# Optimization experiments

Measured on AMD Instinct MI355X. Metric: run time of the kernel, lower is better.

## Reference

```python
import jax, jax.numpy as jnp
import numpy as np

B, F, V, D, K = 16384, 39, 30000, 16, 20
EPS = 1e-5


def bn_eval(x, g, b):
    # inference-mode BatchNorm1d with running_mean=0, running_var=1
    return g * x / jnp.sqrt(1.0 + EPS) + b


def setup_inputs() -> dict:
    key = jax.random.key(0)
    ks = jax.random.split(key, 12)
    x = jax.random.randint(ks[0], (B, F), 0, V)
    emb_table = jax.random.normal(ks[1], (F * V, D), dtype=jnp.float32) * 0.05
    w_c = jax.random.normal(ks[2], (F, F * D), dtype=jnp.float32) * 0.05
    w0 = jax.random.normal(ks[3], (1024, F * D), dtype=jnp.float32) * 0.04
    w1 = jax.random.normal(ks[4], (512, 1024), dtype=jnp.float32) * 0.03
    w_out = jax.random.normal(ks[5], (1, 512), dtype=jnp.float32) * 0.04
    return {
        'x': x, 'emb_table': emb_table,
        'w_c': w_c, 'b_c': jnp.zeros((F,)), 'g_c': jnp.ones((F,)), 'be_c': jnp.zeros((F,)),
        'w0': w0, 'b0': jnp.zeros((1024,)), 'g0': jnp.ones((1024,)), 'be0': jnp.zeros((1024,)),
        'w1': w1, 'b1': jnp.zeros((512,)), 'g1': jnp.ones((512,)), 'be1': jnp.zeros((512,)),
        'w_out': w_out, 'b_out': jnp.zeros((1,)),
    }


def reference(x, emb_table, w_c, b_c, g_c, be_c, w0, b0, g0, be0,
              w1, b1, g1, be1, w_out, b_out):
    offsets = jnp.arange(F, dtype=x.dtype) * V          # per-field offsets
    idx = x + offsets[None, :]                          # [B, F]
    emb = emb_table[idx]                                # [B, F, D] gather

    # controller_mlp: flatten (batch, D, F) layout like torch transpose(1,2)
    flat = jnp.transpose(emb, (0, 2, 1)).reshape(B, F * D)
    h = jax.nn.relu(bn_eval(flat @ w_c.T + b_c, g_c, be_c))
    scores = jax.nn.softmax(h, axis=1)                  # [B, F]

    # kmax_pooling: top-k field indices, sorted ascending, gather weights
    _, kidx = jax.lax.top_k(scores, K)
    kidx = jnp.sort(kidx, axis=1)                       # [B, K]
    w = jnp.take_along_axis(scores, kidx, axis=1)       # [B, K]

    # forward_select: gather selected field embeddings, weight them
    sel = jnp.take_along_axis(emb, kidx[:, :, None], axis=1)  # [B, K, D]
    weighted = sel * w[:, :, None]

    # scatter back into full field slots (unselected fields are zero)
    full = jnp.zeros((B, F, D), weighted.dtype)
    bidx = jnp.arange(B)[:, None]
    full = full.at[bidx, kidx].set(weighted)            # [B, F, D]

    z = jnp.transpose(full, (0, 2, 1)).reshape(B, F * D)
    z = jax.nn.relu(bn_eval(z @ w0.T + b0, g0, be0))
    z = jax.nn.relu(bn_eval(z @ w1.T + b1, g1, be1))
    out = jax.nn.sigmoid(z @ w_out.T + b_out)           # [B, 1]
    return out.squeeze(-1)
```

## Files before the change

### kernel.cpp

```cpp
#include <hip/hip_runtime.h>
#include <math.h>

#define B_SZ 16384
#define F_N 39
#define V_N 30000
#define D_N 16
#define K_SEL 20
#define FD 624
#define KP0 640
#define NCP 48
#define N0 1024
#define N1 512
#define CBR 16
#define ALD 648

typedef unsigned short u16;
typedef __attribute__((ext_vector_type(8))) short bf16x8;
typedef __attribute__((ext_vector_type(8))) unsigned short u16x8;
typedef __attribute__((ext_vector_type(4))) float f32x4;
typedef __attribute__((ext_vector_type(4))) unsigned short u16x4;

__device__ __forceinline__ u16 f2bf(float v) {
    union { float f; unsigned u; } x; x.f = v;
    unsigned r = x.u + 0x7fff + ((x.u >> 16) & 1);
    return (u16)(r >> 16);
}
__device__ __forceinline__ float bf2f(u16 v) {
    union { unsigned u; float f; } x; x.u = ((unsigned)v) << 16;
    return x.f;
}
__device__ __forceinline__ unsigned cvtpk2(float a, float b) {
    unsigned d;
    asm("v_cvt_pk_bf16_f32 %0, %1, %2" : "=v"(d) : "v"(a), "v"(b));
    return d;
}

#define GLD16(gp, lp) __builtin_amdgcn_global_load_lds( \
    (const __attribute__((address_space(1))) unsigned int*)(gp), \
    (__attribute__((address_space(3))) unsigned int*)(lp), 16, 0, 0)

__global__ __launch_bounds__(256) void prep_all_kernel(
    const float* __restrict__ w0, const float* __restrict__ w1,
    const float* __restrict__ w_c, const float* __restrict__ b_c,
    const float* __restrict__ g_c, const float* __restrict__ be_c,
    u16* __restrict__ w0b, u16* __restrict__ w1b, u16* __restrict__ wcb,
    float* __restrict__ bcp, float* __restrict__ gcp, float* __restrict__ becp,
    float* __restrict__ outp)
{
    __shared__ float Lb[8][624];
    const int bid = blockIdx.x;
    const int t   = threadIdx.x;

    if (bid < 134) {
        const bool is_w0 = (bid < 128);
        const int r0 = is_w0 ? bid * 8 : (bid - 128) * 8;
        const int nrows_src = is_w0 ? N0 : F_N;
        const float* __restrict__ src = is_w0 ? w0 : w_c;
        u16* __restrict__ dst = is_w0 ? w0b : wcb;

        for (int j = t; j < 8 * 156; j += 256) {
            const int row = j / 156;
            const int c4  = j - row * 156;
            const int n   = r0 + row;
            if (n < nrows_src)
                *(float4*)&Lb[row][c4 * 4] =
                    *(const float4*)&src[(size_t)n * FD + c4 * 4];
        }
        __syncthreads();

        for (int j = t; j < 8 * 320; j += 256) {
            const int row = j / 320;
            const int pr  = j - row * 320;
            const int n   = r0 + row;
            const int k0  = pr * 2;
            float v0 = 0.f, v1 = 0.f;
            if (n < nrows_src) {
                const int d0 = k0 & 15,       f0 = k0 >> 4;
                const int d1 = (k0 + 1) & 15, f1 = (k0 + 1) >> 4;
                if (f0 < F_N) v0 = Lb[row][d0 * F_N + f0];
                if (f1 < F_N) v1 = Lb[row][d1 * F_N + f1];
            }
            *(unsigned*)&dst[(size_t)n * KP0 + k0] = cvtpk2(v0, v1);
        }
        return;
    }
    if (bid < 390) {
        const size_t e0 = (size_t)(bid - 134) * 2048 + t * 8;
        float4 v0 = *(const float4*)(w1 + e0);
        float4 v1 = *(const float4*)(w1 + e0 + 4);
        uint4 o = { cvtpk2(v0.x, v0.y), cvtpk2(v0.z, v0.w),
                    cvtpk2(v1.x, v1.y), cvtpk2(v1.z, v1.w) };
        *(uint4*)(w1b + e0) = o;
        return;
    }
    if (bid < 398) {
        const size_t e0 = (size_t)(bid - 390) * 2048 + t * 8;
        float4 z = {0.f, 0.f, 0.f, 0.f};
        *(float4*)(outp + e0)     = z;
        *(float4*)(outp + e0 + 4) = z;
        return;
    }
    if (t < 3 * NCP) {
        const int which = t / NCP, n = t - which * NCP;
        float v = 0.f;
        if (n < F_N) v = (which == 0) ? b_c[n] : (which == 1) ? g_c[n] : be_c[n];
        ((which == 0) ? bcp : (which == 1) ? gcp : becp)[n] = v;
    }
}

__global__ __launch_bounds__(256) void fused_controller_kernel(
    const int* __restrict__ x, const float* __restrict__ emb_table,
    const u16* __restrict__ wcb, const float* __restrict__ bcp,
    const float* __restrict__ gcp, const float* __restrict__ becp,
    u16* __restrict__ zb)
{
    __shared__ __align__(16) u16 Al[CBR * ALD];
    __shared__ float vv[CBR][49];
    __shared__ f32x4 part[4][64][3];
    __shared__ float selw[CBR][F_N];

    const int t    = threadIdx.x;
    const int wave = t >> 6;
    const int lane = t & 63;
    const int b0   = blockIdx.x * CBR;

    {
        const int p0 = t, p1 = t + 256, p2 = t + 512;
        const int xi0 = x[b0 * F_N + p0];
        const int xi1 = x[b0 * F_N + p1];
        const int xi2 = (p2 < CBR * F_N) ? x[b0 * F_N + p2] : 0;
        const int pp[3] = { p0, p1, p2 };
        const int xx[3] = { xi0, xi1, xi2 };
        #pragma unroll
        for (int s = 0; s < 3; ++s) {
            const int p = pp[s];
            if (p < CBR * F_N) {
                const int row = p / F_N;
                const int f   = p - row * F_N;
                const float4* src =
                    (const float4*)(emb_table + (size_t)(xx[s] + f * V_N) * D_N);
                float4 v0 = src[0], v1 = src[1], v2 = src[2], v3 = src[3];
                uint4 o0 = { cvtpk2(v0.x, v0.y), cvtpk2(v0.z, v0.w),
                             cvtpk2(v1.x, v1.y), cvtpk2(v1.z, v1.w) };
                uint4 o1 = { cvtpk2(v2.x, v2.y), cvtpk2(v2.z, v2.w),
                             cvtpk2(v3.x, v3.y), cvtpk2(v3.z, v3.w) };
                *(uint4*)&Al[row * ALD + f * D_N]     = o0;
                *(uint4*)&Al[row * ALD + f * D_N + 8] = o1;
            }
        }
    }
    __syncthreads();

    const int m = lane & 15;
    const int q = lane >> 4;
    f32x4 acc0 = {}, acc1 = {}, acc2 = {};
    {
        const u16* ap  = &Al[m * ALD + wave * 160 + q * 8];
        const u16* bp0 = wcb + (size_t)(0  + m) * KP0 + wave * 160 + q * 8;
        const u16* bp1 = wcb + (size_t)(16 + m) * KP0 + wave * 160 + q * 8;
        const u16* bp2 = wcb + (size_t)(32 + m) * KP0 + wave * 160 + q * 8;
        #pragma unroll
        for (int k = 0; k < 5; ++k) {
            bf16x8 af = *(const bf16x8*)ap;
            bf16x8 b0 = *(const bf16x8*)bp0;
            bf16x8 b1 = *(const bf16x8*)bp1;
            bf16x8 b2 = *(const bf16x8*)bp2;
            acc0 = __builtin_amdgcn_mfma_f32_16x16x32_bf16(af, b0, acc0, 0, 0, 0);
            acc1 = __builtin_amdgcn_mfma_f32_16x16x32_bf16(af, b1, acc1, 0, 0, 0);
            acc2 = __builtin_amdgcn_mfma_f32_16x16x32_bf16(af, b2, acc2, 0, 0, 0);
            ap += 32; bp0 += 32; bp1 += 32; bp2 += 32;
        }
    }
    part[wave][lane][0] = acc0;
    part[wave][lane][1] = acc1;
    part[wave][lane][2] = acc2;
    __syncthreads();

    {
        f32x4 r0 = part[0][lane][0] + part[1][lane][0] + part[2][lane][0] + part[3][lane][0];
        f32x4 r1 = part[0][lane][1] + part[1][lane][1] + part[2][lane][1] + part[3][lane][1];
        f32x4 r2 = part[0][lane][2] + part[1][lane][2] + part[2][lane][2] + part[3][lane][2];

        const float rs = rsqrtf(1.0f + 1e-5f);
        if (q == wave) {
            #pragma unroll
            for (int j = 0; j < 3; ++j) {
                const f32x4 a = (j == 0) ? r0 : (j == 1) ? r1 : r2;
                const int n = j * 16 + m;
                const float gn = gcp[n] * rs;
                const float bn = becp[n];
                const float bi = bcp[n];
                #pragma unroll
                for (int r = 0; r < 4; ++r)
                    vv[wave * 4 + r][n] = fmaxf(fmaf(gn, a[r] + bi, bn), 0.f);
            }
        }
    }
    __syncthreads();

    {
        const int row = wave * 4 + (lane >> 4);
        const int fl  = lane & 15;
        float e[3] = {0.f, 0.f, 0.f};
        float mloc = -1e30f;
        #pragma unroll
        for (int it = 0; it < 3; ++it) {
            const int f = fl + 16 * it;
            if (f < F_N) { e[it] = vv[row][f]; mloc = fmaxf(mloc, e[it]); }
        }
        mloc = fmaxf(mloc, __shfl_xor(mloc, 1, 64));
        mloc = fmaxf(mloc, __shfl_xor(mloc, 2, 64));
        mloc = fmaxf(mloc, __shfl_xor(mloc, 4, 64));
        mloc = fmaxf(mloc, __shfl_xor(mloc, 8, 64));
        float sloc = 0.f;
        #pragma unroll
        for (int it = 0; it < 3; ++it) {
            const int f = fl + 16 * it;
            if (f < F_N) { e[it] = expf(e[it] - mloc); sloc += e[it]; }
        }
        sloc += __shfl_xor(sloc, 1, 64);
        sloc += __shfl_xor(sloc, 2, 64);
        sloc += __shfl_xor(sloc, 4, 64);
        sloc += __shfl_xor(sloc, 8, 64);
        const float inv = 1.f / sloc;
        #pragma unroll
        for (int it = 0; it < 3; ++it) {
            const int f = fl + 16 * it;
            if (f < F_N) vv[row][f] = e[it];
        }

        int rank[3] = {};
        for (int gg = 0; gg < F_N; ++gg) {
            const float o = vv[row][gg];
            #pragma unroll
            for (int it = 0; it < 3; ++it) {
                const int f = fl + 16 * it;
                if (f < F_N)
                    rank[it] += (o > e[it] || (o == e[it] && gg < f)) ? 1 : 0;
            }
        }
        #pragma unroll
        for (int it = 0; it < 3; ++it) {
            const int f = fl + 16 * it;
            if (f < F_N)
                selw[row][f] = (rank[it] < K_SEL) ? e[it] * inv : 0.f;
        }
    }
    __syncthreads();

    for (int gp = t; gp < CBR * 40; gp += 256) {
        const int row  = gp / 40;
        const int slot = gp - row * 40;
        u16* dst = zb + (size_t)(b0 + row) * KP0 + slot * D_N;
        uint4 o0 = {0u,0u,0u,0u}, o1 = {0u,0u,0u,0u};
        if (slot < F_N) {
            const float w = selw[row][slot];
            u16x8 a0 = *(u16x8*)&Al[row * ALD + slot * D_N];
            u16x8 a1 = *(u16x8*)&Al[row * ALD + slot * D_N + 8];
            o0 = (uint4){ cvtpk2(bf2f(a0[0]) * w, bf2f(a0[1]) * w),
                          cvtpk2(bf2f(a0[2]) * w, bf2f(a0[3]) * w),
                          cvtpk2(bf2f(a0[4]) * w, bf2f(a0[5]) * w),
                          cvtpk2(bf2f(a0[6]) * w, bf2f(a0[7]) * w) };
            o1 = (uint4){ cvtpk2(bf2f(a1[0]) * w, bf2f(a1[1]) * w),
                          cvtpk2(bf2f(a1[2]) * w, bf2f(a1[3]) * w),
                          cvtpk2(bf2f(a1[4]) * w, bf2f(a1[5]) * w),
                          cvtpk2(bf2f(a1[6]) * w, bf2f(a1[7]) * w) };
        }
        *(uint4*)dst       = o0;
        *(uint4*)(dst + 8) = o1;
    }
}

template<int MODE>
__global__ __launch_bounds__(512) void gemm_mfma_bn_relu(
    const u16* __restrict__ A, const u16* __restrict__ W,
    const float* __restrict__ bias, const float* __restrict__ g,
    const float* __restrict__ be, u16* __restrict__ Cout,
    int M, int N, int Kp,
    const float* __restrict__ w_out, float* __restrict__ outp)
{
    __shared__ __align__(16) u16 SM[3 * 12288];

    const int t    = threadIdx.x;
    const int wave = t >> 6;
    const int lane = t & 63;
    const int wm   = wave >> 1, wn = wave & 1;
    const int m0   = blockIdx.x * 256;
    const int n0   = blockIdx.y * 128;

    const int rA0 = t >> 2;
    const int cA0 = (t & 3) ^ ((rA0 >> 1) & 3);
    const int rA1 = 128 + rA0;
    const int cA1 = (t & 3) ^ ((rA1 >> 1) & 3);
    const u16* gA0 = A + (size_t)(m0 + rA0) * Kp + cA0 * 8;
    const u16* gA1 = A + (size_t)(m0 + rA1) * Kp + cA1 * 8;
    const u16* gB  = W + (size_t)(n0 + rA0) * Kp + cA0 * 8;
    const int dA0 = t * 8, dA1 = 4096 + t * 8, dB = 8192 + t * 8;

    const int q    = lane >> 4;
    const int lr16 = lane & 15;

    int aoff[4], boff[4];
    #pragma unroll
    for (int i = 0; i < 4; ++i) {
        int ra = wm * 64 + i * 16 + lr16;
        aoff[i] = ra * 32 + ((q ^ ((ra >> 1) & 3)) * 8);
        int rb = wn * 64 + i * 16 + lr16;
        boff[i] = rb * 32 + ((q ^ ((rb >> 1) & 3)) * 8);
    }

    const int NIT = Kp >> 5;

    GLD16(gA0, SM + dA0);
    GLD16(gA1, SM + dA1);
    GLD16(gB,  SM + dB);
    gA0 += 32; gA1 += 32; gB += 32;
    GLD16(gA0, SM + 12288 + dA0);
    GLD16(gA1, SM + 12288 + dA1);
    GLD16(gB,  SM + 12288 + dB);
    gA0 += 32; gA1 += 32; gB += 32;

    f32x4 acc[4][4] = {};
    int cur = 0, stg = 2;

    for (int it = 0; it < NIT - 1; ++it) {
        asm volatile("s_waitcnt vmcnt(3)" ::: "memory");
        __builtin_amdgcn_s_barrier();
        __builtin_amdgcn_sched_barrier(0);

        const u16* ac = SM + cur * 12288;
        const u16* bc = ac + 8192;

        bf16x8 af0 = *(const bf16x8*)(ac + aoff[0]);
        bf16x8 af1 = *(const bf16x8*)(ac + aoff[1]);
        bf16x8 b0v = *(const bf16x8*)(bc + boff[0]);
        bf16x8 b1v = *(const bf16x8*)(bc + boff[1]);
        bf16x8 b2v = *(const bf16x8*)(bc + boff[2]);
        bf16x8 b3v = *(const bf16x8*)(bc + boff[3]);

        if (it + 2 < NIT) {
            u16* s = SM + stg * 12288;
            GLD16(gA0, s + dA0);
            GLD16(gA1, s + dA1);
            GLD16(gB,  s + dB);
            gA0 += 32; gA1 += 32; gB += 32;
        }

        asm volatile("s_waitcnt lgkmcnt(0)" ::: "memory");
        __builtin_amdgcn_sched_barrier(0);
        __builtin_amdgcn_s_setprio(1);
        acc[0][0] = __builtin_amdgcn_mfma_f32_16x16x32_bf16(af0, b0v, acc[0][0], 0, 0, 0);
        acc[0][1] = __builtin_amdgcn_mfma_f32_16x16x32_bf16(af0, b1v, acc[0][1], 0, 0, 0);
        acc[0][2] = __builtin_amdgcn_mfma_f32_16x16x32_bf16(af0, b2v, acc[0][2], 0, 0, 0);
        acc[0][3] = __builtin_amdgcn_mfma_f32_16x16x32_bf16(af0, b3v, acc[0][3], 0, 0, 0);
        acc[1][0] = __builtin_amdgcn_mfma_f32_16x16x32_bf16(af1, b0v, acc[1][0], 0, 0, 0);
        acc[1][1] = __builtin_amdgcn_mfma_f32_16x16x32_bf16(af1, b1v, acc[1][1], 0, 0, 0);
        acc[1][2] = __builtin_amdgcn_mfma_f32_16x16x32_bf16(af1, b2v, acc[1][2], 0, 0, 0);
        acc[1][3] = __builtin_amdgcn_mfma_f32_16x16x32_bf16(af1, b3v, acc[1][3], 0, 0, 0);
        __builtin_amdgcn_s_setprio(0);
        __builtin_amdgcn_s_barrier();

        bf16x8 af2 = *(const bf16x8*)(ac + aoff[2]);
        bf16x8 af3 = *(const bf16x8*)(ac + aoff[3]);
        asm volatile("s_waitcnt lgkmcnt(0)" ::: "memory");
        __builtin_amdgcn_sched_barrier(0);
        __builtin_amdgcn_s_setprio(1);
        acc[2][0] = __builtin_amdgcn_mfma_f32_16x16x32_bf16(af2, b0v, acc[2][0], 0, 0, 0);
        acc[2][1] = __builtin_amdgcn_mfma_f32_16x16x32_bf16(af2, b1v, acc[2][1], 0, 0, 0);
        acc[2][2] = __builtin_amdgcn_mfma_f32_16x16x32_bf16(af2, b2v, acc[2][2], 0, 0, 0);
        acc[2][3] = __builtin_amdgcn_mfma_f32_16x16x32_bf16(af2, b3v, acc[2][3], 0, 0, 0);
        acc[3][0] = __builtin_amdgcn_mfma_f32_16x16x32_bf16(af3, b0v, acc[3][0], 0, 0, 0);
        acc[3][1] = __builtin_amdgcn_mfma_f32_16x16x32_bf16(af3, b1v, acc[3][1], 0, 0, 0);
        acc[3][2] = __builtin_amdgcn_mfma_f32_16x16x32_bf16(af3, b2v, acc[3][2], 0, 0, 0);
        acc[3][3] = __builtin_amdgcn_mfma_f32_16x16x32_bf16(af3, b3v, acc[3][3], 0, 0, 0);
        __builtin_amdgcn_s_setprio(0);

        cur = (cur == 2) ? 0 : cur + 1;
        stg = (stg == 2) ? 0 : stg + 1;
    }

    asm volatile("s_waitcnt vmcnt(0)" ::: "memory");
    __builtin_amdgcn_s_barrier();
    __builtin_amdgcn_sched_barrier(0);
    {
        const u16* ac = SM + cur * 12288;
        const u16* bc = ac + 8192;
        bf16x8 af[4], bfr[4];
        #pragma unroll
        for (int i = 0; i < 4; ++i) af[i]  = *(const bf16x8*)(ac + aoff[i]);
        #pragma unroll
        for (int j = 0; j < 4; ++j) bfr[j] = *(const bf16x8*)(bc + boff[j]);
        __builtin_amdgcn_s_setprio(1);
        #pragma unroll
        for (int i = 0; i < 4; ++i)
            #pragma unroll
            for (int j = 0; j < 4; ++j)
                acc[i][j] = __builtin_amdgcn_mfma_f32_16x16x32_bf16(
                    af[i], bfr[j], acc[i][j], 0, 0, 0);
        __builtin_amdgcn_s_setprio(0);
    }

    const float rs = rsqrtf(1.0f + 1e-5f);
    if (MODE == 0) {
        __syncthreads();
        u16* Cs = SM;
        #pragma unroll
        for (int j = 0; j < 4; ++j) {
            const int nl = wn * 64 + j * 16 + lr16;
            const int n  = n0 + nl;
            const float bn_g = g[n] * rs;
            const float bn_b = be[n];
            const float bi   = bias[n];
            #pragma unroll
            for (int i = 0; i < 4; ++i) {
                const int mlb = wm * 64 + i * 16 + q * 4;
                float v0 = fmaxf(fmaf(bn_g, acc[i][j][0] + bi, bn_b), 0.f);
                float v1 = fmaxf(fmaf(bn_g, acc[i][j][1] + bi, bn_b), 0.f);
                float v2 = fmaxf(fmaf(bn_g, acc[i][j][2] + bi, bn_b), 0.f);
                float v3 = fmaxf(fmaf(bn_g, acc[i][j][3] + bi, bn_b), 0.f);
                unsigned pA = cvtpk2(v0, v1);
                unsigned pB = cvtpk2(v2, v3);
                Cs[(mlb + 0) * 136 + nl] = (u16)pA;
                Cs[(mlb + 1) * 136 + nl] = (u16)(pA >> 16);
                Cs[(mlb + 2) * 136 + nl] = (u16)pB;
                Cs[(mlb + 3) * 136 + nl] = (u16)(pB >> 16);
            }
        }
        __syncthreads();
        #pragma unroll
        for (int s = 0; s < 8; ++s) {
            const int chunk = s * 512 + t;
            const int row   = chunk >> 4;
            const int col   = (chunk & 15) << 3;
            *(u16x8*)&Cout[(size_t)(m0 + row) * N + n0 + col] =
                *(const u16x8*)&Cs[row * 136 + col];
        }
    } else {
        float s[4][4] = {};
        #pragma unroll
        for (int j = 0; j < 4; ++j) {
            const int n = n0 + wn * 64 + j * 16 + lr16;
            const float bn_g = g[n] * rs;
            const float bn_b = be[n];
            const float bi   = bias[n];
            const float wo   = w_out[n];
            #pragma unroll
            for (int i = 0; i < 4; ++i)
                #pragma unroll
                for (int r = 0; r < 4; ++r) {
                    float v = acc[i][j][r] + bi;
                    v = fmaxf(fmaf(bn_g, v, bn_b), 0.f);
                    s[i][r] = fmaf(v, wo, s[i][r]);
                }
        }
        #pragma unroll
        for (int i = 0; i < 4; ++i)
            #pragma unroll
            for (int r = 0; r < 4; ++r) {
                float v = s[i][r];
                v += __shfl_xor(v, 1, 64);
                v += __shfl_xor(v, 2, 64);
                v += __shfl_xor(v, 4, 64);
                v += __shfl_xor(v, 8, 64);
                s[i][r] = v;
            }
        if (lr16 == 0) {
            #pragma unroll
            for (int i = 0; i < 4; ++i) {
                const int mbase = m0 + wm * 64 + i * 16 + q * 4;
                #pragma unroll
                for (int r = 0; r < 4; ++r)
                    atomicAdd(&outp[mbase + r], s[i][r]);
            }
        }
    }
}

__global__ __launch_bounds__(256) void sigmoid_kernel(
    const float* __restrict__ outp, const float* __restrict__ b_out,
    float* __restrict__ out)
{
    const int b = blockIdx.x * 256 + threadIdx.x;
    out[b] = 1.f / (1.f + expf(-(outp[b] + b_out[0])));
}

extern "C" void kernel_launch(void* const* d_in, const int* in_sizes, int n_in,
                              void* d_out, int out_size, void* d_ws, size_t ws_size,
                              hipStream_t stream)
{
    const int*   x     = (const int*)  d_in[0];
    const float* emb   = (const float*)d_in[1];
    const float* w_c   = (const float*)d_in[2];
    const float* b_c   = (const float*)d_in[3];
    const float* g_c   = (const float*)d_in[4];
    const float* be_c  = (const float*)d_in[5];
    const float* w0    = (const float*)d_in[6];
    const float* b0    = (const float*)d_in[7];
    const float* g0    = (const float*)d_in[8];
    const float* be0   = (const float*)d_in[9];
    const float* w1    = (const float*)d_in[10];
    const float* b1    = (const float*)d_in[11];
    const float* g1    = (const float*)d_in[12];
    const float* be1   = (const float*)d_in[13];
    const float* w_out = (const float*)d_in[14];
    const float* b_out = (const float*)d_in[15];
    float* out = (float*)d_out;

    u16*   zb    = (u16*)d_ws;
    u16*   w0b   = zb    + (size_t)B_SZ * KP0;
    u16*   h0b   = w0b   + (size_t)N0 * KP0;
    u16*   w1b   = h0b   + (size_t)B_SZ * N0;
    u16*   wcb   = w1b   + (size_t)N1 * N0;
    float* outp  = (float*)(wcb + (size_t)NCP * KP0);
    float* bcp   = outp + B_SZ;
    float* gcp   = bcp + NCP;
    float* becp  = gcp + NCP;

    prep_all_kernel<<<399, 256, 0, stream>>>(
        w0, w1, w_c, b_c, g_c, be_c, w0b, w1b, wcb, bcp, gcp, becp, outp);

    fused_controller_kernel<<<B_SZ / CBR, 256, 0, stream>>>(
        x, emb, wcb, bcp, gcp, becp, zb);

    gemm_mfma_bn_relu<0><<<dim3(B_SZ / 256, N0 / 128), 512, 0, stream>>>(
        zb, w0b, b0, g0, be0, h0b, B_SZ, N0, KP0, nullptr, nullptr);

    gemm_mfma_bn_relu<1><<<dim3(B_SZ / 256, N1 / 128), 512, 0, stream>>>(
        h0b, w1b, b1, g1, be1, nullptr, B_SZ, N1, N0, w_out, outp);

    sigmoid_kernel<<<B_SZ / 256, 256, 0, stream>>>(outp, b_out, out);
}
```

Before: 205.6 us.

## Widen controller tile to 64 rows per block and reshape GEMM tiles to 128x256

The fused controller kernel now handles 64 batch rows per block. Each wave owns 16 rows and runs the full K reduction itself, which removes the cross-wave partial-sum buffer and most block-wide barriers. Embedding gathers are issued ten per thread, with the index loads hoisted ahead of them. The two MLP GEMMs switch from 256x128 to 128x256 output tiles, loading one A tile and two B tiles per stage, with a wider LDS staging stride in the epilogue. The controller change raises LDS use per block to roughly 105 KB, which lowers occupancy and leaves 256 blocks for the whole batch. The MODE 1 epilogue must also stay correct now that four waves, not two, split the N dimension.

```diff
diff --git a/kernel.cpp b/kernel.cpp
--- a/kernel.cpp
+++ b/kernel.cpp
@@ -11,14 +11,13 @@
 #define NCP 48
 #define N0 1024
 #define N1 512
-#define CBR 16
+#define CBR 64
 #define ALD 648
 
 typedef unsigned short u16;
 typedef __attribute__((ext_vector_type(8))) short bf16x8;
 typedef __attribute__((ext_vector_type(8))) unsigned short u16x8;
 typedef __attribute__((ext_vector_type(4))) float f32x4;
-typedef __attribute__((ext_vector_type(4))) unsigned short u16x4;
 
 __device__ __forceinline__ u16 f2bf(float v) {
     union { float f; unsigned u; } x; x.f = v;
@@ -116,7 +115,6 @@
 {
     __shared__ __align__(16) u16 Al[CBR * ALD];
     __shared__ float vv[CBR][49];
-    __shared__ f32x4 part[4][64][3];
     __shared__ float selw[CBR][F_N];
 
     const int t    = threadIdx.x;
@@ -125,20 +123,20 @@
     const int b0   = blockIdx.x * CBR;
 
     {
-        const int p0 = t, p1 = t + 256, p2 = t + 512;
-        const int xi0 = x[b0 * F_N + p0];
-        const int xi1 = x[b0 * F_N + p1];
-        const int xi2 = (p2 < CBR * F_N) ? x[b0 * F_N + p2] : 0;
-        const int pp[3] = { p0, p1, p2 };
-        const int xx[3] = { xi0, xi1, xi2 };
-        #pragma unroll
-        for (int s = 0; s < 3; ++s) {
-            const int p = pp[s];
+        int xi[10];
+        #pragma unroll
+        for (int s = 0; s < 10; ++s) {
+            const int p = t + s * 256;
+            xi[s] = (p < CBR * F_N) ? x[b0 * F_N + p] : 0;
+        }
+        #pragma unroll
+        for (int s = 0; s < 10; ++s) {
+            const int p = t + s * 256;
             if (p < CBR * F_N) {
                 const int row = p / F_N;
                 const int f   = p - row * F_N;
                 const float4* src =
-                    (const float4*)(emb_table + (size_t)(xx[s] + f * V_N) * D_N);
+                    (const float4*)(emb_table + (size_t)(xi[s] + f * V_N) * D_N);
                 float4 v0 = src[0], v1 = src[1], v2 = src[2], v3 = src[3];
                 uint4 o0 = { cvtpk2(v0.x, v0.y), cvtpk2(v0.z, v0.w),
                              cvtpk2(v1.x, v1.y), cvtpk2(v1.z, v1.w) };
@@ -153,14 +151,15 @@
 
     const int m = lane & 15;
     const int q = lane >> 4;
+    const int rbase = wave * 16;
     f32x4 acc0 = {}, acc1 = {}, acc2 = {};
     {
-        const u16* ap  = &Al[m * ALD + wave * 160 + q * 8];
-        const u16* bp0 = wcb + (size_t)(0  + m) * KP0 + wave * 160 + q * 8;
-        const u16* bp1 = wcb + (size_t)(16 + m) * KP0 + wave * 160 + q * 8;
-        const u16* bp2 = wcb + (size_t)(32 + m) * KP0 + wave * 160 + q * 8;
-        #pragma unroll
-        for (int k = 0; k < 5; ++k) {
+        const u16* ap  = &Al[(rbase + m) * ALD + q * 8];
+        const u16* bp0 = wcb + (size_t)(0  + m) * KP0 + q * 8;
+        const u16* bp1 = wcb + (size_t)(16 + m) * KP0 + q * 8;
+        const u16* bp2 = wcb + (size_t)(32 + m) * KP0 + q * 8;
+        #pragma unroll
+        for (int k = 0; k < 20; ++k) {
             bf16x8 af = *(const bf16x8*)ap;
             bf16x8 b0 = *(const bf16x8*)bp0;
             bf16x8 b1 = *(const bf16x8*)bp1;
@@ -171,35 +170,24 @@
             ap += 32; bp0 += 32; bp1 += 32; bp2 += 32;
         }
     }
-    part[wave][lane][0] = acc0;
-    part[wave][lane][1] = acc1;
-    part[wave][lane][2] = acc2;
-    __syncthreads();
 
     {
-        f32x4 r0 = part[0][lane][0] + part[1][lane][0] + part[2][lane][0] + part[3][lane][0];
-        f32x4 r1 = part[0][lane][1] + part[1][lane][1] + part[2][lane][1] + part[3][lane][1];
-        f32x4 r2 = part[0][lane][2] + part[1][lane][2] + part[2][lane][2] + part[3][lane][2];
-
         const float rs = rsqrtf(1.0f + 1e-5f);
-        if (q == wave) {
-            #pragma unroll
-            for (int j = 0; j < 3; ++j) {
-                const f32x4 a = (j == 0) ? r0 : (j == 1) ? r1 : r2;
-                const int n = j * 16 + m;
-                const float gn = gcp[n] * rs;
-                const float bn = becp[n];
-                const float bi = bcp[n];
-                #pragma unroll
-                for (int r = 0; r < 4; ++r)
-                    vv[wave * 4 + r][n] = fmaxf(fmaf(gn, a[r] + bi, bn), 0.f);
-            }
-        }
-    }
-    __syncthreads();
-
-    {
-        const int row = wave * 4 + (lane >> 4);
+        #pragma unroll
+        for (int j = 0; j < 3; ++j) {
+            const f32x4 a = (j == 0) ? acc0 : (j == 1) ? acc1 : acc2;
+            const int n = j * 16 + m;
+            const float gn = gcp[n] * rs;
+            const float bn = becp[n];
+            const float bi = bcp[n];
+            #pragma unroll
+            for (int r = 0; r < 4; ++r)
+                vv[rbase + q * 4 + r][n] = fmaxf(fmaf(gn, a[r] + bi, bn), 0.f);
+        }
+    }
+
+    for (int pass = 0; pass < 4; ++pass) {
+        const int row = rbase + pass * 4 + (lane >> 4);
         const int fl  = lane & 15;
         float e[3] = {0.f, 0.f, 0.f};
         float mloc = -1e30f;
@@ -246,17 +234,17 @@
                 selw[row][f] = (rank[it] < K_SEL) ? e[it] * inv : 0.f;
         }
     }
-    __syncthreads();
-
-    for (int gp = t; gp < CBR * 40; gp += 256) {
+
+    for (int gp = lane; gp < 16 * 40; gp += 64) {
         const int row  = gp / 40;
         const int slot = gp - row * 40;
-        u16* dst = zb + (size_t)(b0 + row) * KP0 + slot * D_N;
+        const int gr   = rbase + row;
+        u16* dst = zb + (size_t)(b0 + gr) * KP0 + slot * D_N;
         uint4 o0 = {0u,0u,0u,0u}, o1 = {0u,0u,0u,0u};
         if (slot < F_N) {
-            const float w = selw[row][slot];
-            u16x8 a0 = *(u16x8*)&Al[row * ALD + slot * D_N];
-            u16x8 a1 = *(u16x8*)&Al[row * ALD + slot * D_N + 8];
+            const float w = selw[gr][slot];
+            u16x8 a0 = *(u16x8*)&Al[gr * ALD + slot * D_N];
+            u16x8 a1 = *(u16x8*)&Al[gr * ALD + slot * D_N + 8];
             o0 = (uint4){ cvtpk2(bf2f(a0[0]) * w, bf2f(a0[1]) * w),
                           cvtpk2(bf2f(a0[2]) * w, bf2f(a0[3]) * w),
                           cvtpk2(bf2f(a0[4]) * w, bf2f(a0[5]) * w),
@@ -284,18 +272,18 @@
     const int t    = threadIdx.x;
     const int wave = t >> 6;
     const int lane = t & 63;
-    const int wm   = wave >> 1, wn = wave & 1;
-    const int m0   = blockIdx.x * 256;
-    const int n0   = blockIdx.y * 128;
-
-    const int rA0 = t >> 2;
-    const int cA0 = (t & 3) ^ ((rA0 >> 1) & 3);
-    const int rA1 = 128 + rA0;
-    const int cA1 = (t & 3) ^ ((rA1 >> 1) & 3);
-    const u16* gA0 = A + (size_t)(m0 + rA0) * Kp + cA0 * 8;
-    const u16* gA1 = A + (size_t)(m0 + rA1) * Kp + cA1 * 8;
-    const u16* gB  = W + (size_t)(n0 + rA0) * Kp + cA0 * 8;
-    const int dA0 = t * 8, dA1 = 4096 + t * 8, dB = 8192 + t * 8;
+    const int wm   = wave >> 2, wn = wave & 3;
+    const int m0   = blockIdx.x * 128;
+    const int n0   = blockIdx.y * 256;
+
+    const int rA  = t >> 2;
+    const int cA  = (t & 3) ^ ((rA >> 1) & 3);
+    const int rB1 = 128 + rA;
+    const int cB1 = (t & 3) ^ ((rB1 >> 1) & 3);
+    const u16* gA  = A + (size_t)(m0 + rA)  * Kp + cA  * 8;
+    const u16* gB0 = W + (size_t)(n0 + rA)  * Kp + cA  * 8;
+    const u16* gB1 = W + (size_t)(n0 + rB1) * Kp + cB1 * 8;
+    const int dA = t * 8, dB0 = 4096 + t * 8, dB1 = 8192 + t * 8;
 
     const int q    = lane >> 4;
     const int lr16 = lane & 15;
@@ -306,19 +294,19 @@
         int ra = wm * 64 + i * 16 + lr16;
         aoff[i] = ra * 32 + ((q ^ ((ra >> 1) & 3)) * 8);
         int rb = wn * 64 + i * 16 + lr16;
-        boff[i] = rb * 32 + ((q ^ ((rb >> 1) & 3)) * 8);
+        boff[i] = 4096 + rb * 32 + ((q ^ ((rb >> 1) & 3)) * 8);
     }
 
     const int NIT = Kp >> 5;
 
-    GLD16(gA0, SM + dA0);
-    GLD16(gA1, SM + dA1);
-    GLD16(gB,  SM + dB);
-    gA0 += 32; gA1 += 32; gB += 32;
-    GLD16(gA0, SM + 12288 + dA0);
-    GLD16(gA1, SM + 12288 + dA1);
-    GLD16(gB,  SM + 12288 + dB);
-    gA0 += 32; gA1 += 32; gB += 32;
+    GLD16(gA,  SM + dA);
+    GLD16(gB0, SM + dB0);
+    GLD16(gB1, SM + dB1);
+    gA += 32; gB0 += 32; gB1 += 32;
+    GLD16(gA,  SM + 12288 + dA);
+    GLD16(gB0, SM + 12288 + dB0);
+    GLD16(gB1, SM + 12288 + dB1);
+    gA += 32; gB0 += 32; gB1 += 32;
 
     f32x4 acc[4][4] = {};
     int cur = 0, stg = 2;
@@ -329,21 +317,20 @@
         __builtin_amdgcn_sched_barrier(0);
 
         const u16* ac = SM + cur * 12288;
-        const u16* bc = ac + 8192;
 
         bf16x8 af0 = *(const bf16x8*)(ac + aoff[0]);
         bf16x8 af1 = *(const bf16x8*)(ac + aoff[1]);
-        bf16x8 b0v = *(const bf16x8*)(bc + boff[0]);
-        bf16x8 b1v = *(const bf16x8*)(bc + boff[1]);
-        bf16x8 b2v = *(const bf16x8*)(bc + boff[2]);
-        bf16x8 b3v = *(const bf16x8*)(bc + boff[3]);
+        bf16x8 b0v = *(const bf16x8*)(ac + boff[0]);
+        bf16x8 b1v = *(const bf16x8*)(ac + boff[1]);
+        bf16x8 b2v = *(const bf16x8*)(ac + boff[2]);
+        bf16x8 b3v = *(const bf16x8*)(ac + boff[3]);
 
         if (it + 2 < NIT) {
             u16* s = SM + stg * 12288;
-            GLD16(gA0, s + dA0);
-            GLD16(gA1, s + dA1);
-            GLD16(gB,  s + dB);
-            gA0 += 32; gA1 += 32; gB += 32;
+            GLD16(gA,  s + dA);
+            GLD16(gB0, s + dB0);
+            GLD16(gB1, s + dB1);
+            gA += 32; gB0 += 32; gB1 += 32;
         }
 
         asm volatile("s_waitcnt lgkmcnt(0)" ::: "memory");
@@ -384,12 +371,11 @@
     __builtin_amdgcn_sched_barrier(0);
     {
         const u16* ac = SM + cur * 12288;
-        const u16* bc = ac + 8192;
         bf16x8 af[4], bfr[4];
         #pragma unroll
         for (int i = 0; i < 4; ++i) af[i]  = *(const bf16x8*)(ac + aoff[i]);
         #pragma unroll
-        for (int j = 0; j < 4; ++j) bfr[j] = *(const bf16x8*)(bc + boff[j]);
+        for (int j = 0; j < 4; ++j) bfr[j] = *(const bf16x8*)(ac + boff[j]);
         __builtin_amdgcn_s_setprio(1);
         #pragma unroll
         for (int i = 0; i < 4; ++i)
@@ -420,20 +406,20 @@
                 float v3 = fmaxf(fmaf(bn_g, acc[i][j][3] + bi, bn_b), 0.f);
                 unsigned pA = cvtpk2(v0, v1);
                 unsigned pB = cvtpk2(v2, v3);
-                Cs[(mlb + 0) * 136 + nl] = (u16)pA;
-                Cs[(mlb + 1) * 136 + nl] = (u16)(pA >> 16);
-                Cs[(mlb + 2) * 136 + nl] = (u16)pB;
-                Cs[(mlb + 3) * 136 + nl] = (u16)(pB >> 16);
+                Cs[(mlb + 0) * 264 + nl] = (u16)pA;
+                Cs[(mlb + 1) * 264 + nl] = (u16)(pA >> 16);
+                Cs[(mlb + 2) * 264 + nl] = (u16)pB;
+                Cs[(mlb + 3) * 264 + nl] = (u16)(pB >> 16);
             }
         }
         __syncthreads();
         #pragma unroll
         for (int s = 0; s < 8; ++s) {
             const int chunk = s * 512 + t;
-            const int row   = chunk >> 4;
-            const int col   = (chunk & 15) << 3;
+            const int row   = chunk >> 5;
+            const int col   = (chunk & 31) << 3;
             *(u16x8*)&Cout[(size_t)(m0 + row) * N + n0 + col] =
-                *(const u16x8*)&Cs[row * 136 + col];
+                *(const u16x8*)&Cs[row * 264 + col];
         }
     } else {
         float s[4][4] = {};
@@ -522,10 +508,10 @@
     fused_controller_kernel<<<B_SZ / CBR, 256, 0, stream>>>(
         x, emb, wcb, bcp, gcp, becp, zb);
 
-    gemm_mfma_bn_relu<0><<<dim3(B_SZ / 256, N0 / 128), 512, 0, stream>>>(
+    gemm_mfma_bn_relu<0><<<dim3(B_SZ / 128, N0 / 256), 512, 0, stream>>>(
         zb, w0b, b0, g0, be0, h0b, B_SZ, N0, KP0, nullptr, nullptr);
 
-    gemm_mfma_bn_relu<1><<<dim3(B_SZ / 256, N1 / 128), 512, 0, stream>>>(
+    gemm_mfma_bn_relu<1><<<dim3(B_SZ / 128, N1 / 256), 512, 0, stream>>>(
         h0b, w1b, b1, g1, be1, nullptr, B_SZ, N1, N0, w_out, outp);
 
     sigmoid_kernel<<<B_SZ / 256, 256, 0, stream>>>(outp, b_out, out);
```

Result: slower. 223.1 us (+8.5%).
